# Kernel optimization log

Hardware: AMD Instinct MI355X
Metric: run time of the kernel (lower is better)

The kernel has to match this reference:

```python
import jax, jax.numpy as jnp
import numpy as np

N, E = 20000, 160000
NFEAT, NHID, NCLASS = 512, 256, 64


def _unif(key, shape):
    s = 1.0 / np.sqrt(shape[-1])
    return jax.random.uniform(key, shape, jnp.float32, -s, s)


def setup_inputs() -> dict:
    key = jax.random.key(0)
    ks = jax.random.split(key, 16)
    return {
        "x": jax.random.normal(ks[0], (N, NFEAT), jnp.float32),
        "edge_index": jax.random.randint(ks[1], (2, E), 0, N, dtype=jnp.int32).astype(jnp.int64),
        "head": 0,
        # Relation 1 (nfeat -> nfeat)
        "r1_g1": _unif(ks[2], (NFEAT, NFEAT)),
        "r1_g2": _unif(ks[3], (NFEAT, NFEAT)),
        "r1_b1": _unif(ks[4], (NFEAT, NFEAT)),
        "r1_b2": _unif(ks[5], (NFEAT, NFEAT)),
        "r1_m": _unif(ks[6], (1, NFEAT)),
        "gc1_w": _unif(ks[7], (NHID, NFEAT)),   # GCNConv.lin.weight [out,in]
        "gc1_b": jnp.zeros((NHID,), jnp.float32),
        # Relation 2 (nhid -> nhid)
        "r2_g1": _unif(ks[8], (NHID, NHID)),
        "r2_g2": _unif(ks[9], (NHID, NHID)),
        "r2_b1": _unif(ks[10], (NHID, NHID)),
        "r2_b2": _unif(ks[11], (NHID, NHID)),
        "r2_m": _unif(ks[12], (1, NHID)),
        "gc2_w": _unif(ks[13], (NCLASS, NHID)),
        "gc2_b": jnp.zeros((NCLASS,), jnp.float32),
    }


def _scatter_mean(vals, idx, n):
    s = jax.ops.segment_sum(vals, idx, num_segments=n)
    c = jax.ops.segment_sum(jnp.ones(idx.shape, vals.dtype), idx, num_segments=n)
    return s / jnp.clip(c, 1.0)[:, None]


def _relation(ft, nb, g1, g2, b1, b2, m):
    # gamma/beta FiLM-style modulation, then TransE-style translation
    gamma = jax.nn.leaky_relu(ft @ g1.T + nb @ g2.T, 0.2) + 1.0
    beta = jax.nn.leaky_relu(ft @ b1.T + nb @ b2.T, 0.2)
    return ft + (gamma * m + beta) - nb


def _gcn(x, edge_index, w, b):
    # PyG GCNConv with add_self_loops=True, symmetric normalization
    n = x.shape[0]
    h = x @ w.T
    loop = jnp.arange(n, dtype=edge_index.dtype)
    row = jnp.concatenate([edge_index[0], loop])
    col = jnp.concatenate([edge_index[1], loop])
    deg = jax.ops.segment_sum(jnp.ones(col.shape, h.dtype), col, num_segments=n)
    dinv = jnp.where(deg > 0, deg ** -0.5, 0.0)
    norm = dinv[row] * dinv[col]
    out = jax.ops.segment_sum(norm[:, None] * h[row], col, num_segments=n)
    return out + b


def _trans_gcn(x, edge_index, rg1, rg2, rb1, rb2, rm, gw, gb, head):
    row, col = edge_index[0], edge_index[1]
    n = x.shape[0]
    num_nb = jax.ops.segment_sum(jnp.ones(row.shape, x.dtype), row, num_segments=n)
    nb = _scatter_mean(x[col], row, n)
    output = _relation(x, nb, rg1, rg2, rb1, rb2, rm)
    h_k = _gcn(x, edge_index, gw, gb)
    if not head:  # tail branch (ablation=0: h_s = output)
        h_s = output @ gw.T
        h_k = (h_k + h_s) / (num_nb + 1.0)[:, None]
    return h_k, output


def reference(x, edge_index, head, r1_g1, r1_g2, r1_b1, r1_b2, r1_m, gc1_w, gc1_b,
              r2_g1, r2_g2, r2_b1, r2_b2, r2_m, gc2_w, gc2_b):
    x1, out1 = _trans_gcn(x, edge_index, r1_g1, r1_g2, r1_b1, r1_b2, r1_m, gc1_w, gc1_b, head)
    x1 = jax.nn.elu(x1)  # dropout is identity in eval mode
    x2, out2 = _trans_gcn(x1, edge_index, r2_g1, r2_g2, r2_b1, r2_b2, r2_m, gc2_w, gc2_b, head)
    return (x2, jax.nn.log_softmax(x2, axis=1), out1, out2)
```

## Files before the change

kernel.cpp:

```cpp
#include <hip/hip_runtime.h>
#include <hip/hip_bf16.h>
#include <stdint.h>

typedef __bf16 bf16;
typedef __attribute__((ext_vector_type(8))) __bf16 bf16x8;
typedef __attribute__((ext_vector_type(4))) float f32x4;

#define NNODE 20000
#define NEDGE 160000
#define NFEATD 512
#define NHIDD 256
#define NCLSD 64

__device__ __forceinline__ void async_copy16(const bf16* g, bf16* l) {
  __builtin_amdgcn_global_load_lds((__attribute__((address_space(1))) void*)g,
                                   (__attribute__((address_space(3))) void*)l,
                                   16, 0, 0);
}

struct GemmArgs {
  const bf16 *A1, *A2, *W1, *W2, *zpage;
  int ldA, ldW, K1, Ktot, Nvalid, ldC, Nrows, Arows, Wrows;
  bf16* outB;
  float* outF;
  float* outF2;
  const float* mrow;
  const float* Xf;
  const bf16* Xh;
  const bf16* nbm;
  float* outG;
  bf16* outB2;
  const float* agg;
  const bf16* hself;
  int hld;
  const float* dinv;
  const float* bias;
  const float* rnb;
  int elu;
  const bf16* Wh;
  int ldWh, Wrowsh, Kh, Nintmain;
};

template <int MODE>
__global__ __launch_bounds__(256) void gemm_bt(GemmArgs ga) {
  __shared__ bf16 sA[2][128 * 64];
  __shared__ bf16 sB[2][128 * 64];
  const int tid = threadIdx.x;
  const int lane = tid & 63;
  const int w = tid >> 6;
  const int wm = w >> 1, wn = w & 1;

  const int gx = gridDim.x;
  const int nwg = gx * gridDim.y;
  const int orig = blockIdx.y * gx + blockIdx.x;
  const int qq = nwg >> 3, rm = nwg & 7;
  const int xcd = orig & 7, sidx = orig >> 3;
  const int wg = (xcd < rm ? xcd * (qq + 1) : rm * (qq + 1) + (xcd - rm) * qq) + sidx;
  const int bn0 = (wg % gx) * 128;
  const int bm0 = (wg / gx) * 128;

  const bool isH = (MODE == 2) && ga.Wh && (bn0 >= ga.Nintmain);
  const bf16* Wp1 = isH ? ga.Wh : ga.W1;
  const bf16* Wp2 = isH ? ga.Wh : ga.W2;
  const int ldW = isH ? ga.ldWh : ga.ldW;
  const int Wrows = isH ? ga.Wrowsh : ga.Wrows;
  const int bn0L = isH ? bn0 - ga.Nintmain : bn0;
  const int nt1 = (isH ? ga.Kh : ga.K1) >> 6;
  const int nt = (isH ? ga.Kh : ga.Ktot) >> 6;

  const int srow = tid >> 3;
  const int scol = (((tid & 7) ^ (srow & 7)) << 3);
  const bf16* zp = ga.zpage + tid * 8;
  int offA[4], offB[4];
  bool okA[4], okB[4];
#pragma unroll
  for (int r = 0; r < 4; r++) {
    const int ra = bm0 + r * 32 + srow;
    const int rb = bn0L + r * 32 + srow;
    okA[r] = ra < ga.Arows;
    okB[r] = rb < Wrows;
    offA[r] = ra * ga.ldA + scol;
    offB[r] = rb * ldW + scol;
  }

  auto stage = [&](int t, int p) {
    const int seg = t >= nt1;
    const int koff = (t - (seg ? nt1 : 0)) << 6;
    const bf16* As = seg ? ga.A2 : ga.A1;
    const bf16* Ws = seg ? Wp2 : Wp1;
    bf16* dA = &sA[p][tid * 8];
    bf16* dB = &sB[p][tid * 8];
#pragma unroll
    for (int r = 0; r < 4; r++)
      async_copy16(okA[r] ? As + offA[r] + koff : zp, dA + r * 2048);
#pragma unroll
    for (int r = 0; r < 4; r++)
      async_copy16(okB[r] ? Ws + offB[r] + koff : zp, dB + r * 2048);
  };

  const int sl = lane >> 4;
  const int rAb = wm * 64 + (lane & 15);
  const int rBb = wn * 64 + (lane & 15);
  const int a7 = rAb & 7, b7 = rBb & 7;

  f32x4 acc[4][4] = {};

  stage(0, 0);
  stage(1, 1);
  asm volatile("s_waitcnt vmcnt(8)" ::: "memory");
  __builtin_amdgcn_s_barrier();
  asm volatile("" ::: "memory");

  for (int t = 0; t < nt; ++t) {
    const int p = t & 1;
    const bf16* pA = &sA[p][0];
    const bf16* pB = &sB[p][0];
    bf16x8 af[4][2], bv[4][2];
#pragma unroll
    for (int mi = 0; mi < 4; mi++)
#pragma unroll
      for (int kk = 0; kk < 2; kk++)
        af[mi][kk] = *(const bf16x8*)((const char*)pA + (rAb + mi * 16) * 128 +
                                      ((((kk << 2) + sl) ^ a7) << 4));
#pragma unroll
    for (int ni = 0; ni < 4; ni++)
#pragma unroll
      for (int kk = 0; kk < 2; kk++)
        bv[ni][kk] = *(const bf16x8*)((const char*)pB + (rBb + ni * 16) * 128 +
                                      ((((kk << 2) + sl) ^ b7) << 4));
    if (t + 2 < nt) {
      asm volatile("s_waitcnt lgkmcnt(0)" ::: "memory");
      __builtin_amdgcn_s_barrier();
      asm volatile("" ::: "memory");
      stage(t + 2, p);
    }
    __builtin_amdgcn_s_setprio(1);
#pragma unroll
    for (int mi = 0; mi < 4; mi++)
#pragma unroll
      for (int ni = 0; ni < 4; ni++)
#pragma unroll
        for (int kk = 0; kk < 2; kk++)
          acc[mi][ni] =
              __builtin_amdgcn_mfma_f32_16x16x32_bf16(af[mi][kk], bv[ni][kk], acc[mi][ni], 0, 0, 0);
    __builtin_amdgcn_s_setprio(0);
    if (t + 1 < nt) {
      if (t + 2 < nt) asm volatile("s_waitcnt vmcnt(8)" ::: "memory");
      else            asm volatile("s_waitcnt vmcnt(0)" ::: "memory");
      __builtin_amdgcn_s_barrier();
      asm volatile("" ::: "memory");
    }
  }

  if constexpr (MODE == 0) {
    const int Nv = ga.Nvalid;
#pragma unroll
    for (int mi = 0; mi < 4; mi++) {
      const int rb = bm0 + wm * 64 + mi * 16 + ((lane >> 4) << 2);
#pragma unroll
      for (int ni = 0; ni < 4; ni++) {
        const int c = bn0 + wn * 64 + ni * 16 + (lane & 15);
#pragma unroll
        for (int i = 0; i < 4; i++) {
          const int r = rb + i;
          if (r < ga.Nrows && c < Nv) ga.outB[(size_t)r * ga.ldC + c] = (bf16)acc[mi][ni][i];
        }
      }
    }
  } else if constexpr (MODE == 2) {
    if (isH) {
#pragma unroll
      for (int mi = 0; mi < 4; mi++) {
        const int rb = bm0 + wm * 64 + mi * 16 + ((lane >> 4) << 2);
#pragma unroll
        for (int ni = 0; ni < 4; ni++) {
          const int c = bn0L + wn * 64 + ni * 16 + (lane & 15);
#pragma unroll
          for (int i = 0; i < 4; i++) {
            const int r = rb + i;
            if (r < ga.Nrows && c < ga.ldC) ga.outB[(size_t)r * ga.ldC + c] = (bf16)acc[mi][ni][i];
          }
        }
      }
    } else {
      const int Dr = ga.Nvalid;
      const int Lb = ((bn0 + wn * 64) >> 1) + (lane & 15);
#pragma unroll
      for (int mi = 0; mi < 4; mi++) {
        const int rb = bm0 + wm * 64 + mi * 16 + ((lane >> 4) << 2);
#pragma unroll
        for (int p = 0; p < 2; p++) {
          const int L = Lb + p * 16;
          const float mv = ga.mrow[L];
#pragma unroll
          for (int i = 0; i < 4; i++) {
            const int r = rb + i;
            if (r >= ga.Nrows) continue;
            const size_t idx = (size_t)r * Dr + L;
            float vg = acc[mi][2 * p][i];
            float vb = acc[mi][2 * p + 1][i];
            float gamma = (vg > 0.f ? vg : 0.2f * vg) + 1.0f;
            float beta = vb > 0.f ? vb : 0.2f * vb;
            float ft = ga.Xf ? ga.Xf[idx] : (float)ga.Xh[idx];
            float o = ft + gamma * mv + beta - (float)ga.nbm[idx];
            ga.outG[idx] = o;
            ga.outB2[idx] = (bf16)o;
          }
        }
      }
    }
  } else if constexpr (MODE == 3) {
    const int Nv = ga.Nvalid;
#pragma unroll
    for (int mi = 0; mi < 4; mi++) {
      const int rb = bm0 + wm * 64 + mi * 16 + ((lane >> 4) << 2);
#pragma unroll
      for (int ni = 0; ni < 4; ni++) {
        const int c = bn0 + wn * 64 + ni * 16 + (lane & 15);
#pragma unroll
        for (int i = 0; i < 4; i++) {
          const int r = rb + i;
          if (r >= ga.Nrows || c >= Nv) continue;
          const size_t idx = (size_t)r * ga.ldC + c;
          float dv = ga.dinv[r];
          float hs = (float)ga.hself[(size_t)r * ga.hld + c];
          float hv = (ga.agg[idx] + dv * dv * hs + ga.bias[c] + acc[mi][ni][i]) * ga.rnb[r];
          if (ga.elu) hv = hv > 0.f ? hv : expm1f(hv);
          ga.outB[idx] = (bf16)hv;
        }
      }
    }
  } else {
    if (wn == 0) {
#pragma unroll
      for (int mi = 0; mi < 4; mi++) {
        const int rb = bm0 + wm * 64 + mi * 16 + ((lane >> 4) << 2);
#pragma unroll
        for (int i = 0; i < 4; i++) {
          const int r = rb + i;
          const bool ok = r < ga.Nrows;
          float dv = ok ? ga.dinv[r] : 0.f;
          float rn = ok ? ga.rnb[r] : 1.f;
          float hv[4];
#pragma unroll
          for (int ni = 0; ni < 4; ni++) {
            const int c = ni * 16 + (lane & 15);
            float hs = ok ? (float)ga.hself[(size_t)r * ga.hld + c] : 0.f;
            float ag = ok ? ga.agg[(size_t)r * 64 + c] : 0.f;
            hv[ni] = ok ? (ag + dv * dv * hs + ga.bias[c] + acc[mi][ni][i]) * rn : 0.f;
          }
          float mx = fmaxf(fmaxf(hv[0], hv[1]), fmaxf(hv[2], hv[3]));
          mx = fmaxf(mx, __shfl_xor(mx, 1));
          mx = fmaxf(mx, __shfl_xor(mx, 2));
          mx = fmaxf(mx, __shfl_xor(mx, 4));
          mx = fmaxf(mx, __shfl_xor(mx, 8));
          float s = expf(hv[0] - mx) + expf(hv[1] - mx) + expf(hv[2] - mx) + expf(hv[3] - mx);
          s += __shfl_xor(s, 1);
          s += __shfl_xor(s, 2);
          s += __shfl_xor(s, 4);
          s += __shfl_xor(s, 8);
          float ls = logf(s);
          if (ok) {
#pragma unroll
            for (int ni = 0; ni < 4; ni++) {
              const int c = ni * 16 + (lane & 15);
              ga.outF[(size_t)r * 64 + c] = hv[ni];
              ga.outF2[(size_t)r * 64 + c] = hv[ni] - mx - ls;
            }
          }
        }
      }
    }
  }
}

#define PREP_NB0 10000
#define PREP_NB1 10128
#define PREP_NB2 10144
#define PREP_NB3 11168
#define PREP_NB4 11424
#define PREP_NB5 11589

__device__ __forceinline__ void cvt4(const float* __restrict__ src, bf16* __restrict__ dst,
                                     int i) {
  float4 v = *(const float4*)(src + i);
  union { bf16 b[4]; uint2 u; } o;
  o.b[0] = (bf16)v.x; o.b[1] = (bf16)v.y; o.b[2] = (bf16)v.z; o.b[3] = (bf16)v.w;
  *(uint2*)(dst + i) = o.u;
}

__device__ __forceinline__ void relw4(const float* __restrict__ g1, const float* __restrict__ g2,
                                      const float* __restrict__ b1, const float* __restrict__ b2,
                                      bf16* __restrict__ dst, int D, int idx) {
  int R = idx / (2 * D), C = idx % (2 * D);
  int q = R >> 5, s = R & 31;
  int sr = q * 16 + (s & 15);
  const float* src = (s < 16) ? ((C < D) ? g1 : g2) : ((C < D) ? b1 : b2);
  int cc = (C < D) ? C : C - D;
  float4 v = *(const float4*)(src + (size_t)sr * D + cc);
  union { bf16 b[4]; uint2 u; } o;
  o.b[0] = (bf16)v.x; o.b[1] = (bf16)v.y; o.b[2] = (bf16)v.z; o.b[3] = (bf16)v.w;
  *(uint2*)(dst + (size_t)R * 2 * D + C) = o.u;
}

__global__ __launch_bounds__(256) void prep_all(
    const float* __restrict__ x, const float* __restrict__ gc1w, const float* __restrict__ gc2w,
    const float* __restrict__ r1g1, const float* __restrict__ r1g2,
    const float* __restrict__ r1b1, const float* __restrict__ r1b2,
    const float* __restrict__ r2g1, const float* __restrict__ r2g2,
    const float* __restrict__ r2b1, const float* __restrict__ r2b2,
    bf16* __restrict__ xb, bf16* __restrict__ wgc1, bf16* __restrict__ wgc2,
    bf16* __restrict__ Wrel1, bf16* __restrict__ Wrel2,
    int* __restrict__ icr, int* __restrict__ icc, int* __restrict__ zpage) {
  const int b = blockIdx.x;
  const int tid = threadIdx.x;
  if (b < PREP_NB0) {
    cvt4(x, xb, (b * 256 + tid) * 4);
  } else if (b < PREP_NB1) {
    cvt4(gc1w, wgc1, ((b - PREP_NB0) * 256 + tid) * 4);
  } else if (b < PREP_NB2) {
    cvt4(gc2w, wgc2, ((b - PREP_NB1) * 256 + tid) * 4);
  } else if (b < PREP_NB3) {
    relw4(r1g1, r1g2, r1b1, r1b2, Wrel1, 512, ((b - PREP_NB2) * 256 + tid) * 4);
  } else if (b < PREP_NB4) {
    relw4(r2g1, r2g2, r2b1, r2b2, Wrel2, 256, ((b - PREP_NB3) * 256 + tid) * 4);
  } else {
    int i = (b - PREP_NB4) * 256 + tid;
    if (i < NNODE) icr[i] = 0;
    else if (i < 2 * NNODE) icc[i - NNODE] = 0;
    else if (i < 2 * NNODE + 2048) zpage[i - 2 * NNODE] = 0;
  }
}

__global__ void count_int(const int* __restrict__ ei, int* cr, int* cc, int E) {
  int e = blockIdx.x * 256 + threadIdx.x;
  if (e < E) {
    atomicAdd(&cr[ei[e]], 1);
    atomicAdd(&cc[ei[E + e]], 1);
  }
}

__global__ void scan_excl2(const int* __restrict__ cr, const int* __restrict__ cc,
                           int* __restrict__ rptr, int* __restrict__ cptr,
                           int* __restrict__ curr, int* __restrict__ curc,
                           float* __restrict__ nbscale, float* __restrict__ rnb,
                           float* __restrict__ dinv, int n) {
  int t = threadIdx.x;
  {
    int b0 = blockIdx.x * (n / 2);
    for (int j = b0 + t; j < b0 + n / 2; j += 256) {
      float a = (float)cr[j];
      nbscale[j] = 1.0f / fmaxf(a, 1.0f);
      rnb[j] = 1.0f / (a + 1.0f);
      dinv[j] = rsqrtf((float)cc[j] + 1.0f);
    }
  }
  const int* cnt = blockIdx.x ? cc : cr;
  int* ptr = blockIdx.x ? cptr : rptr;
  int* cur = blockIdx.x ? curc : curr;
  __shared__ int part[256];
  int chunk = (n + 255) / 256;
  int base = t * chunk;
  int s = 0;
  for (int i = 0; i < chunk; i++) {
    int j = base + i;
    if (j < n) s += cnt[j];
  }
  part[t] = s;
  __syncthreads();
  if (t == 0) {
    int r = 0;
    for (int i = 0; i < 256; i++) { int v = part[i]; part[i] = r; r += v; }
    ptr[n] = r;
  }
  __syncthreads();
  int run = part[t];
  for (int i = 0; i < chunk; i++) {
    int j = base + i;
    if (j < n) {
      ptr[j] = run;
      cur[j] = run;
      run += cnt[j];
    }
  }
}

__global__ void csr_fill(const int* __restrict__ ei, int* cur_r, int* cur_c,
                         int* __restrict__ adj_r, int* __restrict__ adj_c, int E) {
  int e = blockIdx.x * 256 + threadIdx.x;
  if (e >= E) return;
  int row = ei[e], col = ei[E + e];
  int p = atomicAdd(&cur_r[row], 1);
  adj_r[p] = col;
  int q = atomicAdd(&cur_c[col], 1);
  adj_c[q] = row;
}

__global__ void spmm_nb1(const int* __restrict__ rowptr, const int* __restrict__ adj,
                         const bf16* __restrict__ x, const float* __restrict__ nbscale,
                         bf16* __restrict__ nbp, int n) {
  int r = blockIdx.x * 4 + (threadIdx.x >> 6);
  if (r >= n) return;
  int lane = threadIdx.x & 63;
  int e0 = rowptr[r], e1 = rowptr[r + 1];
  float a[8] = {0.f, 0.f, 0.f, 0.f, 0.f, 0.f, 0.f, 0.f};
  int e = e0;
  for (; e + 8 <= e1; e += 8) {
    union { uint4 u; bf16 b[8]; } v[8];
    int ix[8];
#pragma unroll
    for (int k = 0; k < 8; k++) ix[k] = adj[e + k];
#pragma unroll
    for (int k = 0; k < 8; k++) v[k].u = *(const uint4*)(x + (size_t)ix[k] * NFEATD + lane * 8);
#pragma unroll
    for (int j = 0; j < 8; j++) {
      float t = 0.f;
#pragma unroll
      for (int k = 0; k < 8; k++) t += (float)v[k].b[j];
      a[j] += t;
    }
  }
  for (; e + 4 <= e1; e += 4) {
    int i0 = adj[e], i1 = adj[e + 1], i2 = adj[e + 2], i3 = adj[e + 3];
    union { uint4 u; bf16 b[8]; } v0, v1, v2, v3;
    v0.u = *(const uint4*)(x + (size_t)i0 * NFEATD + lane * 8);
    v1.u = *(const uint4*)(x + (size_t)i1 * NFEATD + lane * 8);
    v2.u = *(const uint4*)(x + (size_t)i2 * NFEATD + lane * 8);
    v3.u = *(const uint4*)(x + (size_t)i3 * NFEATD + lane * 8);
#pragma unroll
    for (int j = 0; j < 8; j++)
      a[j] += (float)v0.b[j] + (float)v1.b[j] + (float)v2.b[j] + (float)v3.b[j];
  }
  for (; e < e1; e++) {
    union { uint4 u; bf16 b[8]; } v;
    v.u = *(const uint4*)(x + (size_t)adj[e] * NFEATD + lane * 8);
#pragma unroll
    for (int j = 0; j < 8; j++) a[j] += (float)v.b[j];
  }
  float s = nbscale[r];
  union { bf16 b[8]; uint4 u; } o;
#pragma unroll
  for (int j = 0; j < 8; j++) o.b[j] = (bf16)(a[j] * s);
  *(uint4*)(nbp + (size_t)r * NFEATD + lane * 8) = o.u;
}

__global__ void spmm_nb2(const int* __restrict__ rowptr, const int* __restrict__ adj,
                         const bf16* __restrict__ x, const float* __restrict__ nbscale,
                         bf16* __restrict__ nbp, int n) {
  int r = blockIdx.x * 4 + (threadIdx.x >> 6);
  if (r >= n) return;
  int lane = threadIdx.x & 63;
  int e0 = rowptr[r], e1 = rowptr[r + 1];
  float a[4] = {0.f, 0.f, 0.f, 0.f};
  int e = e0;
  for (; e + 8 <= e1; e += 8) {
    union { uint2 u; bf16 b[4]; } v[8];
    int ix[8];
#pragma unroll
    for (int k = 0; k < 8; k++) ix[k] = adj[e + k];
#pragma unroll
    for (int k = 0; k < 8; k++) v[k].u = *(const uint2*)(x + (size_t)ix[k] * NHIDD + lane * 4);
#pragma unroll
    for (int j = 0; j < 4; j++) {
      float t = 0.f;
#pragma unroll
      for (int k = 0; k < 8; k++) t += (float)v[k].b[j];
      a[j] += t;
    }
  }
  for (; e + 4 <= e1; e += 4) {
    int i0 = adj[e], i1 = adj[e + 1], i2 = adj[e + 2], i3 = adj[e + 3];
    union { uint2 u; bf16 b[4]; } v0, v1, v2, v3;
    v0.u = *(const uint2*)(x + (size_t)i0 * NHIDD + lane * 4);
    v1.u = *(const uint2*)(x + (size_t)i1 * NHIDD + lane * 4);
    v2.u = *(const uint2*)(x + (size_t)i2 * NHIDD + lane * 4);
    v3.u = *(const uint2*)(x + (size_t)i3 * NHIDD + lane * 4);
#pragma unroll
    for (int j = 0; j < 4; j++)
      a[j] += (float)v0.b[j] + (float)v1.b[j] + (float)v2.b[j] + (float)v3.b[j];
  }
  for (; e < e1; e++) {
    union { uint2 u; bf16 b[4]; } v;
    v.u = *(const uint2*)(x + (size_t)adj[e] * NHIDD + lane * 4);
#pragma unroll
    for (int j = 0; j < 4; j++) a[j] += (float)v.b[j];
  }
  float s = nbscale[r];
  union { bf16 b[4]; uint2 u; } o;
#pragma unroll
  for (int j = 0; j < 4; j++) o.b[j] = (bf16)(a[j] * s);
  *(uint2*)(nbp + (size_t)r * NHIDD + lane * 4) = o.u;
}

__global__ void spmm_gcn256(const int* __restrict__ colptr, const int* __restrict__ adj,
                            const bf16* __restrict__ h, int hld, const float* __restrict__ dinv,
                            float* __restrict__ agg, int n) {
  int c = blockIdx.x * 4 + (threadIdx.x >> 6);
  if (c >= n) return;
  int lane = threadIdx.x & 63;
  int e0 = colptr[c], e1 = colptr[c + 1];
  float a[4] = {0.f, 0.f, 0.f, 0.f};
  int e = e0;
  for (; e + 4 <= e1; e += 4) {
    int i0 = adj[e], i1 = adj[e + 1], i2 = adj[e + 2], i3 = adj[e + 3];
    float w0 = dinv[i0], w1 = dinv[i1], w2 = dinv[i2], w3 = dinv[i3];
    union { uint2 u; bf16 b[4]; } v0, v1, v2, v3;
    v0.u = *(const uint2*)(h + (size_t)i0 * hld + lane * 4);
    v1.u = *(const uint2*)(h + (size_t)i1 * hld + lane * 4);
    v2.u = *(const uint2*)(h + (size_t)i2 * hld + lane * 4);
    v3.u = *(const uint2*)(h + (size_t)i3 * hld + lane * 4);
#pragma unroll
    for (int j = 0; j < 4; j++)
      a[j] += w0 * (float)v0.b[j] + w1 * (float)v1.b[j] + w2 * (float)v2.b[j] + w3 * (float)v3.b[j];
  }
  for (; e < e1; e++) {
    int rr = adj[e];
    float wv = dinv[rr];
    union { uint2 u; bf16 b[4]; } v;
    v.u = *(const uint2*)(h + (size_t)rr * hld + lane * 4);
#pragma unroll
    for (int j = 0; j < 4; j++) a[j] += wv * (float)v.b[j];
  }
  float wc = dinv[c];
  f32x4 o;
#pragma unroll
  for (int j = 0; j < 4; j++) o[j] = a[j] * wc;
  *(f32x4*)(agg + (size_t)c * NHIDD + lane * 4) = o;
}

__global__ void spmm_gcn64(const int* __restrict__ colptr, const int* __restrict__ adj,
                           const bf16* __restrict__ h, int hld, const float* __restrict__ dinv,
                           float* __restrict__ agg, int n) {
  int c = blockIdx.x * 4 + (threadIdx.x >> 6);
  if (c >= n) return;
  int lane = threadIdx.x & 63;
  int e0 = colptr[c], e1 = colptr[c + 1];
  float a = 0.f;
  int e = e0;
  for (; e + 4 <= e1; e += 4) {
    int i0 = adj[e], i1 = adj[e + 1], i2 = adj[e + 2], i3 = adj[e + 3];
    float h0 = (float)h[(size_t)i0 * hld + lane];
    float h1 = (float)h[(size_t)i1 * hld + lane];
    float h2 = (float)h[(size_t)i2 * hld + lane];
    float h3 = (float)h[(size_t)i3 * hld + lane];
    a += dinv[i0] * h0 + dinv[i1] * h1 + dinv[i2] * h2 + dinv[i3] * h3;
  }
  for (; e < e1; e++) {
    int rr = adj[e];
    a += dinv[rr] * (float)h[(size_t)rr * hld + lane];
  }
  agg[(size_t)c * NCLSD + lane] = a * dinv[c];
}

extern "C" void kernel_launch(void* const* d_in, const int* in_sizes, int n_in, void* d_out,
                              int out_size, void* d_ws, size_t ws_size, hipStream_t stream) {
  const float* x = (const float*)d_in[0];
  const int* ei = (const int*)d_in[1];
  const float* r1g1 = (const float*)d_in[3];
  const float* r1g2 = (const float*)d_in[4];
  const float* r1b1 = (const float*)d_in[5];
  const float* r1b2 = (const float*)d_in[6];
  const float* r1m = (const float*)d_in[7];
  const float* gc1w = (const float*)d_in[8];
  const float* gc1b = (const float*)d_in[9];
  const float* r2g1 = (const float*)d_in[10];
  const float* r2g2 = (const float*)d_in[11];
  const float* r2b1 = (const float*)d_in[12];
  const float* r2b2 = (const float*)d_in[13];
  const float* r2m = (const float*)d_in[14];
  const float* gc2w = (const float*)d_in[15];
  const float* gc2b = (const float*)d_in[16];
  float* out = (float*)d_out;

  char* ws = (char*)d_ws;
  size_t off = 0;
  auto alloc = [&](size_t bytes) -> char* {
    char* p = ws + off;
    off = (off + bytes + 511) & ~(size_t)511;
    return p;
  };
  float* nbscale = (float*)alloc((size_t)NNODE * 4);
  float* rnb = (float*)alloc((size_t)NNODE * 4);
  float* dinv = (float*)alloc((size_t)NNODE * 4);
  int* icr = (int*)alloc((size_t)NNODE * 4);
  int* icc = (int*)alloc((size_t)NNODE * 4);
  int* rptr = (int*)alloc((size_t)(NNODE + 1) * 4);
  int* cptr = (int*)alloc((size_t)(NNODE + 1) * 4);
  int* curr = (int*)alloc((size_t)NNODE * 4);
  int* curc = (int*)alloc((size_t)NNODE * 4);
  int* adjr = (int*)alloc((size_t)NEDGE * 4);
  int* adjc = (int*)alloc((size_t)NEDGE * 4);
  bf16* zpage = (bf16*)alloc(8192);
  bf16* Wrel1 = (bf16*)alloc((size_t)1024 * 1024 * 2);
  bf16* Wrel2 = (bf16*)alloc((size_t)512 * 512 * 2);
  bf16* wgc1 = (bf16*)alloc((size_t)NHIDD * NFEATD * 2);
  bf16* wgc2 = (bf16*)alloc((size_t)NCLSD * NHIDD * 2);
  bf16* xb = (bf16*)alloc((size_t)NNODE * NFEATD * 2);
  bf16* nbp1 = (bf16*)alloc((size_t)NNODE * NFEATD * 2);
  bf16* out1b = (bf16*)alloc((size_t)NNODE * NFEATD * 2);
  bf16* h1b = (bf16*)alloc((size_t)NNODE * NHIDD * 2);
  float* agg1 = (float*)alloc((size_t)NNODE * NHIDD * 4);
  bf16* x1b = (bf16*)alloc((size_t)NNODE * NHIDD * 2);
  bf16* nb2p = (bf16*)alloc((size_t)NNODE * NHIDD * 2);
  bf16* out2b = (bf16*)alloc((size_t)NNODE * NHIDD * 2);
  bf16* h2b = (bf16*)alloc((size_t)NNODE * NCLSD * 2);
  float* agg2 = (float*)alloc((size_t)NNODE * NCLSD * 4);

  const size_t OUT1OFF = (size_t)2 * NNODE * NCLSD;
  const size_t OUT2OFF = OUT1OFF + (size_t)NNODE * NFEATD;
  float* out1g = out + OUT1OFF;
  float* out2g = out + OUT2OFF;

  const int MB = (NNODE + 127) / 128;
  const int NW4 = (NNODE + 3) / 4;

  prep_all<<<PREP_NB5, 256, 0, stream>>>(x, gc1w, gc2w, r1g1, r1g2, r1b1, r1b2,
                                         r2g1, r2g2, r2b1, r2b2, xb, wgc1, wgc2,
                                         Wrel1, Wrel2, icr, icc, (int*)zpage);

  count_int<<<(NEDGE + 255) / 256, 256, 0, stream>>>(ei, icr, icc, NEDGE);
  scan_excl2<<<2, 256, 0, stream>>>(icr, icc, rptr, cptr, curr, curc, nbscale, rnb, dinv, NNODE);
  csr_fill<<<(NEDGE + 255) / 256, 256, 0, stream>>>(ei, curr, curc, adjr, adjc, NEDGE);

  spmm_nb1<<<NW4, 256, 0, stream>>>(rptr, adjr, xb, nbscale, nbp1, NNODE);

  GemmArgs a;
  auto base = [&](const bf16* A1, const bf16* A2, int ldA, const bf16* W1, const bf16* W2,
                  int ldW, int K1, int Kt, int Nv, int ldC, int Wr) {
    a = GemmArgs{};
    a.A1 = A1; a.A2 = A2; a.W1 = W1; a.W2 = W2; a.zpage = zpage;
    a.ldA = ldA; a.ldW = ldW; a.K1 = K1; a.Ktot = Kt; a.Nvalid = Nv; a.ldC = ldC;
    a.Nrows = NNODE; a.Arows = NNODE; a.Wrows = Wr;
  };

  base(xb, nbp1, NFEATD, Wrel1, Wrel1 + 512, 1024, NFEATD, 2 * NFEATD, NFEATD, NHIDD, 1024);
  a.mrow = r1m; a.Xf = x; a.nbm = nbp1; a.outG = out1g; a.outB2 = out1b;
  a.Wh = wgc1; a.ldWh = NFEATD; a.Wrowsh = NHIDD; a.Kh = NFEATD; a.Nintmain = 1024;
  a.outB = h1b;
  gemm_bt<2><<<dim3(10, MB), 256, 0, stream>>>(a);

  spmm_gcn256<<<NW4, 256, 0, stream>>>(cptr, adjc, h1b, NHIDD, dinv, agg1, NNODE);

  base(out1b, out1b, NFEATD, wgc1, wgc1, NFEATD, NFEATD, NFEATD, NHIDD, NHIDD, NHIDD);
  a.agg = agg1; a.hself = h1b; a.hld = NHIDD; a.dinv = dinv; a.bias = gc1b; a.rnb = rnb;
  a.elu = 1; a.outB = x1b;
  gemm_bt<3><<<dim3(2, MB), 256, 0, stream>>>(a);

  spmm_nb2<<<NW4, 256, 0, stream>>>(rptr, adjr, x1b, nbscale, nb2p, NNODE);

  base(x1b, nb2p, NHIDD, Wrel2, Wrel2 + 256, 512, NHIDD, 2 * NHIDD, NHIDD, NCLSD, 512);
  a.mrow = r2m; a.Xf = nullptr; a.Xh = x1b; a.nbm = nb2p; a.outG = out2g; a.outB2 = out2b;
  a.Wh = wgc2; a.ldWh = NHIDD; a.Wrowsh = NCLSD; a.Kh = NHIDD; a.Nintmain = 512;
  a.outB = h2b;
  gemm_bt<2><<<dim3(5, MB), 256, 0, stream>>>(a);

  spmm_gcn64<<<NW4, 256, 0, stream>>>(cptr, adjc, h2b, NCLSD, dinv, agg2, NNODE);

  base(out2b, out2b, NHIDD, wgc2, wgc2, NHIDD, NHIDD, NHIDD, NCLSD, NCLSD, NCLSD);
  a.agg = agg2; a.hself = h2b; a.hld = NCLSD; a.dinv = dinv; a.bias = gc2b; a.rnb = rnb;
  a.elu = 0; a.outF = out; a.outF2 = out + (size_t)NNODE * NCLSD;
  gemm_bt<4><<<dim3(1, MB), 256, 0, stream>>>(a);
}
```

Measured before the change: 493.6 us.

## Fuse GCN neighbor aggregation SpMM into epilogue of GCN output GEMMs

Removes the standalone spmm_gcn256 and spmm_gcn64 kernels and their fp32 aggregation buffers. Each GEMM workgroup now gathers the normalized neighbor sum for its 128-row tile into reused shared memory before the epilogue, then reads it from LDS instead of global memory. This saves two launches and a write-and-read round trip of the fp32 aggregate. In exchange the gather is serialized in the GEMM tail with limited parallelism per workgroup, which could lengthen those kernels.

```diff
diff --git a/kernel.cpp b/kernel.cpp
--- a/kernel.cpp
+++ b/kernel.cpp
@@ -30,7 +30,6 @@
   const bf16* nbm;
   float* outG;
   bf16* outB2;
-  const float* agg;
   const bf16* hself;
   int hld;
   const float* dinv;
@@ -39,12 +38,15 @@
   int elu;
   const bf16* Wh;
   int ldWh, Wrowsh, Kh, Nintmain;
+  const int* gptr;
+  const int* gadj;
 };
 
 template <int MODE>
 __global__ __launch_bounds__(256) void gemm_bt(GemmArgs ga) {
-  __shared__ bf16 sA[2][128 * 64];
-  __shared__ bf16 sB[2][128 * 64];
+  __shared__ bf16 smem[4 * 128 * 64];
+  bf16 (*sA)[128 * 64] = reinterpret_cast<bf16(*)[128 * 64]>(smem);
+  bf16 (*sB)[128 * 64] = reinterpret_cast<bf16(*)[128 * 64]>(smem + 2 * 128 * 64);
   const int tid = threadIdx.x;
   const int lane = tid & 63;
   const int w = tid >> 6;
@@ -210,34 +212,124 @@
       }
     }
   } else if constexpr (MODE == 3) {
+    float (*aggL)[128] = reinterpret_cast<float (*)[128]>(smem);
+    __syncthreads();
+    {
+      const int rg = lane >> 4;
+      const int cl = lane & 15;
+      const bf16* hb = ga.hself;
+      for (int g = 0; g < 8; g++) {
+        const int rl = w * 32 + g * 4 + rg;
+        const int r = bm0 + rl;
+        float a[8] = {};
+        if (r < ga.Nrows) {
+          const int e1 = ga.gptr[r + 1];
+          int e = ga.gptr[r];
+          for (; e + 4 <= e1; e += 4) {
+            int i0 = ga.gadj[e], i1 = ga.gadj[e + 1], i2 = ga.gadj[e + 2], i3 = ga.gadj[e + 3];
+            float w0 = ga.dinv[i0], w1 = ga.dinv[i1], w2 = ga.dinv[i2], w3 = ga.dinv[i3];
+            union { uint4 u; bf16 b[8]; } v0, v1, v2, v3;
+            v0.u = *(const uint4*)(hb + (size_t)i0 * ga.hld + bn0 + cl * 8);
+            v1.u = *(const uint4*)(hb + (size_t)i1 * ga.hld + bn0 + cl * 8);
+            v2.u = *(const uint4*)(hb + (size_t)i2 * ga.hld + bn0 + cl * 8);
+            v3.u = *(const uint4*)(hb + (size_t)i3 * ga.hld + bn0 + cl * 8);
+#pragma unroll
+            for (int j = 0; j < 8; j++)
+              a[j] += w0 * (float)v0.b[j] + w1 * (float)v1.b[j] +
+                      w2 * (float)v2.b[j] + w3 * (float)v3.b[j];
+          }
+          for (; e < e1; e++) {
+            int i0 = ga.gadj[e];
+            float w0 = ga.dinv[i0];
+            union { uint4 u; bf16 b[8]; } v0;
+            v0.u = *(const uint4*)(hb + (size_t)i0 * ga.hld + bn0 + cl * 8);
+#pragma unroll
+            for (int j = 0; j < 8; j++) a[j] += w0 * (float)v0.b[j];
+          }
+          const float dr = ga.dinv[r];
+#pragma unroll
+          for (int j = 0; j < 8; j++) a[j] *= dr;
+        }
+        f32x4 lo = {a[0], a[1], a[2], a[3]}, hi = {a[4], a[5], a[6], a[7]};
+        *(f32x4*)&aggL[rl][cl * 8] = lo;
+        *(f32x4*)&aggL[rl][cl * 8 + 4] = hi;
+      }
+    }
+    __syncthreads();
     const int Nv = ga.Nvalid;
 #pragma unroll
     for (int mi = 0; mi < 4; mi++) {
-      const int rb = bm0 + wm * 64 + mi * 16 + ((lane >> 4) << 2);
+      const int lrb = wm * 64 + mi * 16 + ((lane >> 4) << 2);
 #pragma unroll
       for (int ni = 0; ni < 4; ni++) {
-        const int c = bn0 + wn * 64 + ni * 16 + (lane & 15);
+        const int lc = wn * 64 + ni * 16 + (lane & 15);
+        const int c = bn0 + lc;
 #pragma unroll
         for (int i = 0; i < 4; i++) {
-          const int r = rb + i;
+          const int lr = lrb + i;
+          const int r = bm0 + lr;
           if (r >= ga.Nrows || c >= Nv) continue;
           const size_t idx = (size_t)r * ga.ldC + c;
           float dv = ga.dinv[r];
           float hs = (float)ga.hself[(size_t)r * ga.hld + c];
-          float hv = (ga.agg[idx] + dv * dv * hs + ga.bias[c] + acc[mi][ni][i]) * ga.rnb[r];
+          float hv = (aggL[lr][lc] + dv * dv * hs + ga.bias[c] + acc[mi][ni][i]) * ga.rnb[r];
           if (ga.elu) hv = hv > 0.f ? hv : expm1f(hv);
           ga.outB[idx] = (bf16)hv;
         }
       }
     }
   } else {
+    float (*aggL)[64] = reinterpret_cast<float (*)[64]>(smem);
+    __syncthreads();
+    {
+      const int rg = lane >> 4;
+      const int cl = lane & 15;
+      const bf16* hb = ga.hself;
+      for (int g = 0; g < 8; g++) {
+        const int rl = w * 32 + g * 4 + rg;
+        const int r = bm0 + rl;
+        float a[4] = {};
+        if (r < ga.Nrows) {
+          const int e1 = ga.gptr[r + 1];
+          int e = ga.gptr[r];
+          for (; e + 4 <= e1; e += 4) {
+            int i0 = ga.gadj[e], i1 = ga.gadj[e + 1], i2 = ga.gadj[e + 2], i3 = ga.gadj[e + 3];
+            float w0 = ga.dinv[i0], w1 = ga.dinv[i1], w2 = ga.dinv[i2], w3 = ga.dinv[i3];
+            union { uint2 u; bf16 b[4]; } v0, v1, v2, v3;
+            v0.u = *(const uint2*)(hb + (size_t)i0 * ga.hld + cl * 4);
+            v1.u = *(const uint2*)(hb + (size_t)i1 * ga.hld + cl * 4);
+            v2.u = *(const uint2*)(hb + (size_t)i2 * ga.hld + cl * 4);
+            v3.u = *(const uint2*)(hb + (size_t)i3 * ga.hld + cl * 4);
+#pragma unroll
+            for (int j = 0; j < 4; j++)
+              a[j] += w0 * (float)v0.b[j] + w1 * (float)v1.b[j] +
+                      w2 * (float)v2.b[j] + w3 * (float)v3.b[j];
+          }
+          for (; e < e1; e++) {
+            int i0 = ga.gadj[e];
+            float w0 = ga.dinv[i0];
+            union { uint2 u; bf16 b[4]; } v0;
+            v0.u = *(const uint2*)(hb + (size_t)i0 * ga.hld + cl * 4);
+#pragma unroll
+            for (int j = 0; j < 4; j++) a[j] += w0 * (float)v0.b[j];
+          }
+          const float dr = ga.dinv[r];
+#pragma unroll
+          for (int j = 0; j < 4; j++) a[j] *= dr;
+        }
+        f32x4 v = {a[0], a[1], a[2], a[3]};
+        *(f32x4*)&aggL[rl][cl * 4] = v;
+      }
+    }
+    __syncthreads();
     if (wn == 0) {
 #pragma unroll
       for (int mi = 0; mi < 4; mi++) {
-        const int rb = bm0 + wm * 64 + mi * 16 + ((lane >> 4) << 2);
+        const int lrb = wm * 64 + mi * 16 + ((lane >> 4) << 2);
 #pragma unroll
         for (int i = 0; i < 4; i++) {
-          const int r = rb + i;
+          const int lr = lrb + i;
+          const int r = bm0 + lr;
           const bool ok = r < ga.Nrows;
           float dv = ok ? ga.dinv[r] : 0.f;
           float rn = ok ? ga.rnb[r] : 1.f;
@@ -246,7 +338,7 @@
           for (int ni = 0; ni < 4; ni++) {
             const int c = ni * 16 + (lane & 15);
             float hs = ok ? (float)ga.hself[(size_t)r * ga.hld + c] : 0.f;
-            float ag = ok ? ga.agg[(size_t)r * 64 + c] : 0.f;
+            float ag = ok ? aggL[lr][c] : 0.f;
             hv[ni] = ok ? (ag + dv * dv * hs + ga.bias[c] + acc[mi][ni][i]) * rn : 0.f;
           }
           float mx = fmaxf(fmaxf(hv[0], hv[1]), fmaxf(hv[2], hv[3]));
@@ -490,66 +582,6 @@
 #pragma unroll
   for (int j = 0; j < 4; j++) o.b[j] = (bf16)(a[j] * s);
   *(uint2*)(nbp + (size_t)r * NHIDD + lane * 4) = o.u;
-}
-
-__global__ void spmm_gcn256(const int* __restrict__ colptr, const int* __restrict__ adj,
-                            const bf16* __restrict__ h, int hld, const float* __restrict__ dinv,
-                            float* __restrict__ agg, int n) {
-  int c = blockIdx.x * 4 + (threadIdx.x >> 6);
-  if (c >= n) return;
-  int lane = threadIdx.x & 63;
-  int e0 = colptr[c], e1 = colptr[c + 1];
-  float a[4] = {0.f, 0.f, 0.f, 0.f};
-  int e = e0;
-  for (; e + 4 <= e1; e += 4) {
-    int i0 = adj[e], i1 = adj[e + 1], i2 = adj[e + 2], i3 = adj[e + 3];
-    float w0 = dinv[i0], w1 = dinv[i1], w2 = dinv[i2], w3 = dinv[i3];
-    union { uint2 u; bf16 b[4]; } v0, v1, v2, v3;
-    v0.u = *(const uint2*)(h + (size_t)i0 * hld + lane * 4);
-    v1.u = *(const uint2*)(h + (size_t)i1 * hld + lane * 4);
-    v2.u = *(const uint2*)(h + (size_t)i2 * hld + lane * 4);
-    v3.u = *(const uint2*)(h + (size_t)i3 * hld + lane * 4);
-#pragma unroll
-    for (int j = 0; j < 4; j++)
-      a[j] += w0 * (float)v0.b[j] + w1 * (float)v1.b[j] + w2 * (float)v2.b[j] + w3 * (float)v3.b[j];
-  }
-  for (; e < e1; e++) {
-    int rr = adj[e];
-    float wv = dinv[rr];
-    union { uint2 u; bf16 b[4]; } v;
-    v.u = *(const uint2*)(h + (size_t)rr * hld + lane * 4);
-#pragma unroll
-    for (int j = 0; j < 4; j++) a[j] += wv * (float)v.b[j];
-  }
-  float wc = dinv[c];
-  f32x4 o;
-#pragma unroll
-  for (int j = 0; j < 4; j++) o[j] = a[j] * wc;
-  *(f32x4*)(agg + (size_t)c * NHIDD + lane * 4) = o;
-}
-
-__global__ void spmm_gcn64(const int* __restrict__ colptr, const int* __restrict__ adj,
-                           const bf16* __restrict__ h, int hld, const float* __restrict__ dinv,
-                           float* __restrict__ agg, int n) {
-  int c = blockIdx.x * 4 + (threadIdx.x >> 6);
-  if (c >= n) return;
-  int lane = threadIdx.x & 63;
-  int e0 = colptr[c], e1 = colptr[c + 1];
-  float a = 0.f;
-  int e = e0;
-  for (; e + 4 <= e1; e += 4) {
-    int i0 = adj[e], i1 = adj[e + 1], i2 = adj[e + 2], i3 = adj[e + 3];
-    float h0 = (float)h[(size_t)i0 * hld + lane];
-    float h1 = (float)h[(size_t)i1 * hld + lane];
-    float h2 = (float)h[(size_t)i2 * hld + lane];
-    float h3 = (float)h[(size_t)i3 * hld + lane];
-    a += dinv[i0] * h0 + dinv[i1] * h1 + dinv[i2] * h2 + dinv[i3] * h3;
-  }
-  for (; e < e1; e++) {
-    int rr = adj[e];
-    a += dinv[rr] * (float)h[(size_t)rr * hld + lane];
-  }
-  agg[(size_t)c * NCLSD + lane] = a * dinv[c];
 }
 
 extern "C" void kernel_launch(void* const* d_in, const int* in_sizes, int n_in, void* d_out,
@@ -599,12 +631,10 @@
   bf16* nbp1 = (bf16*)alloc((size_t)NNODE * NFEATD * 2);
   bf16* out1b = (bf16*)alloc((size_t)NNODE * NFEATD * 2);
   bf16* h1b = (bf16*)alloc((size_t)NNODE * NHIDD * 2);
-  float* agg1 = (float*)alloc((size_t)NNODE * NHIDD * 4);
   bf16* x1b = (bf16*)alloc((size_t)NNODE * NHIDD * 2);
   bf16* nb2p = (bf16*)alloc((size_t)NNODE * NHIDD * 2);
   bf16* out2b = (bf16*)alloc((size_t)NNODE * NHIDD * 2);
   bf16* h2b = (bf16*)alloc((size_t)NNODE * NCLSD * 2);
-  float* agg2 = (float*)alloc((size_t)NNODE * NCLSD * 4);
 
   const size_t OUT1OFF = (size_t)2 * NNODE * NCLSD;
   const size_t OUT2OFF = OUT1OFF + (size_t)NNODE * NFEATD;
@@ -639,11 +669,9 @@
   a.outB = h1b;
   gemm_bt<2><<<dim3(10, MB), 256, 0, stream>>>(a);
 
-  spmm_gcn256<<<NW4, 256, 0, stream>>>(cptr, adjc, h1b, NHIDD, dinv, agg1, NNODE);
-
   base(out1b, out1b, NFEATD, wgc1, wgc1, NFEATD, NFEATD, NFEATD, NHIDD, NHIDD, NHIDD);
-  a.agg = agg1; a.hself = h1b; a.hld = NHIDD; a.dinv = dinv; a.bias = gc1b; a.rnb = rnb;
-  a.elu = 1; a.outB = x1b;
+  a.hself = h1b; a.hld = NHIDD; a.dinv = dinv; a.bias = gc1b; a.rnb = rnb;
+  a.elu = 1; a.outB = x1b; a.gptr = cptr; a.gadj = adjc;
   gemm_bt<3><<<dim3(2, MB), 256, 0, stream>>>(a);
 
   spmm_nb2<<<NW4, 256, 0, stream>>>(rptr, adjr, x1b, nbscale, nb2p, NNODE);
@@ -654,10 +682,9 @@
   a.outB = h2b;
   gemm_bt<2><<<dim3(5, MB), 256, 0, stream>>>(a);
 
-  spmm_gcn64<<<NW4, 256, 0, stream>>>(cptr, adjc, h2b, NCLSD, dinv, agg2, NNODE);
-
   base(out2b, out2b, NHIDD, wgc2, wgc2, NHIDD, NHIDD, NHIDD, NCLSD, NCLSD, NCLSD);
-  a.agg = agg2; a.hself = h2b; a.hld = NCLSD; a.dinv = dinv; a.bias = gc2b; a.rnb = rnb;
+  a.hself = h2b; a.hld = NCLSD; a.dinv = dinv; a.bias = gc2b; a.rnb = rnb;
   a.elu = 0; a.outF = out; a.outF2 = out + (size_t)NNODE * NCLSD;
+  a.gptr = cptr; a.gadj = adjc;
   gemm_bt<4><<<dim3(1, MB), 256, 0, stream>>>(a);
 }
```

New measurement: 512.0 us. +3.7%, slower.
